# Kernel tuning notes

Measured on AMD Instinct MI355X. Metric: run time of the kernel, lower is better.

The kernel has to match this reference:

```python
import jax, jax.numpy as jnp
import numpy as np
import math

B, S, STATE, H, D = 4, 2048, 1024, 16, 64
N_ROT = 32  # int(0.5*64), even
ROPE_BASE = 10000.0


def setup_inputs() -> dict:
    key = jax.random.key(0)
    ks = jax.random.split(key, 8)
    q_src = jax.random.normal(ks[0], (B, S, STATE), jnp.float32)
    k_src = jax.random.normal(ks[1], (B, S, STATE), jnp.float32)
    v_src = jax.random.normal(ks[2], (B, S, STATE), jnp.float32)
    # causal position mask: True = masked (torch masked_fill semantics)
    position_mask = jnp.triu(jnp.ones((S, S), jnp.bool_), k=1)
    sd = 0.02
    Wq = jax.random.normal(ks[3], (H * D, STATE), jnp.float32) * sd
    Wk = jax.random.normal(ks[4], (H * D, STATE), jnp.float32) * sd
    Wv = jax.random.normal(ks[5], (H * D, STATE), jnp.float32) * sd
    Wo = jax.random.normal(ks[6], (STATE, H * D), jnp.float32) * sd
    return {"q_src": q_src, "k_src": k_src, "v_src": v_src,
            "position_mask": position_mask,
            "Wq": Wq, "Wk": Wk, "Wv": Wv, "Wo": Wo}


def _rotate_half(x):
    x1, x2 = jnp.split(x, 2, axis=-1)
    return jnp.concatenate([-x2, x1], axis=-1)


def _rope(q, k, offset):
    # q,k: [B,H,S,N_ROT]; positions: k at arange(Sk), q at offset+arange(Sq)
    inv_freq = 1.0 / (ROPE_BASE ** (jnp.arange(0, N_ROT, 2, dtype=jnp.float32) / N_ROT))
    def sincos(pos):
        freqs = pos[:, None] * inv_freq[None, :]          # [S, N_ROT/2]
        emb = jnp.concatenate([freqs, freqs], axis=-1)    # [S, N_ROT]
        return jnp.sin(emb), jnp.cos(emb)
    sk, ck = sincos(jnp.arange(k.shape[-2], dtype=jnp.float32))
    sq, cq = sincos(offset + jnp.arange(q.shape[-2], dtype=jnp.float32))
    q = q * cq + _rotate_half(q) * sq
    k = k * ck + _rotate_half(k) * sk
    return q, k


def reference(q_src, k_src, v_src, position_mask, Wq, Wk, Wv, Wo):
    qk_scale = (1.0 / math.sqrt(D)) ** 0.5  # sqrt of 1/sqrt(D), applied to q and k
    def heads(x):  # [B,S,H*D] -> [B,H,S,D]
        return x.reshape(B, S, H, D).transpose(0, 2, 1, 3)
    q = heads((q_src @ Wq.T) * qk_scale)
    k = heads((k_src @ Wk.T) * qk_scale)
    v = heads(v_src @ Wv.T)
    # inline RoPE on first N_ROT dims (pos_offset = 0, no kv cache)
    rq, rk = _rope(q[..., :N_ROT], k[..., :N_ROT], 0.0)
    q = jnp.concatenate([rq, q[..., N_ROT:]], axis=-1)
    k = jnp.concatenate([rk, k[..., N_ROT:]], axis=-1)
    att = jnp.einsum('bhqd,bhkd->bhqk', q, k)
    att = jnp.where(position_mask[None, None], -jnp.inf, att)
    att = jax.nn.softmax(att, axis=-1)
    out = jnp.einsum('bhqk,bhkd->bhqd', att, v)
    out = out.transpose(0, 2, 1, 3).reshape(B, S, H * D)
    return out @ Wo.T
```

## Files before the change

kernel.cpp:

```cpp
#include <hip/hip_runtime.h>

typedef unsigned short u16;
typedef unsigned int u32;
typedef short short8 __attribute__((ext_vector_type(8)));
typedef float f32x4 __attribute__((ext_vector_type(4)));
typedef float f32x16 __attribute__((ext_vector_type(16)));

#define NB 4
#define NS 2048
#define NSTATE 1024
#define NH 16
#define ND 64
#define NM (NB*NS)

#if __has_builtin(__builtin_amdgcn_exp2f)
#define EXP2(x) __builtin_amdgcn_exp2f(x)
#else
#define EXP2(x) __expf((x) * 0.6931471805599453f)
#endif

__device__ __forceinline__ u16 f2bf(float f){
  union { float fv; unsigned uv; } x; x.fv = f;
  unsigned r = x.uv + 0x7fffu + ((x.uv >> 16) & 1u);
  return (u16)(r >> 16);
}

__device__ __forceinline__ u32 cvtpk(float lo, float hi){
  u32 r;
  asm("v_cvt_pk_bf16_f32 %0, %1, %2" : "=v"(r) : "v"(lo), "v"(hi));
  return r;
}

__device__ __forceinline__ f32x4 mfma16x16(short8 a, short8 b, f32x4 c){
  return __builtin_amdgcn_mfma_f32_16x16x32_bf16(a, b, c, 0, 0, 0);
}

__device__ __forceinline__ f32x16 mfma32(short8 a, short8 b, f32x16 c){
  return __builtin_amdgcn_mfma_f32_32x32x16_bf16(a, b, c, 0, 0, 0);
}

__device__ __forceinline__ void gld_lds16(const u16* g, u16* l){
  __builtin_amdgcn_global_load_lds((const __attribute__((address_space(1))) void*)g,
                                   (__attribute__((address_space(3))) void*)l, 16, 0, 0);
}

__global__ __launch_bounds__(256)
void cvt_all(const float* __restrict__ q, const float* __restrict__ k, const float* __restrict__ v,
             const float* __restrict__ wq, const float* __restrict__ wk,
             const float* __restrict__ wv, const float* __restrict__ wo,
             u16* oq, u16* ok, u16* ov, u16* owq, u16* owk, u16* owv, u16* owo){
  const int XN4 = (NB*NS*NSTATE)/4;
  const int WN4 = (NSTATE*NSTATE)/4;
  int gid = blockIdx.x * 256 + threadIdx.x;
  const float* src; u16* dst; int idx;
  if (gid < XN4)          { src = q; dst = oq; idx = gid; }
  else if (gid < 2*XN4)   { src = k; dst = ok; idx = gid - XN4; }
  else if (gid < 3*XN4)   { src = v; dst = ov; idx = gid - 2*XN4; }
  else {
    int g = gid - 3*XN4;
    int wsel = g >> 18;
    idx = g & (WN4 - 1);
    src = (wsel==0)?wq:(wsel==1)?wk:(wsel==2)?wv:wo;
    dst = (wsel==0)?owq:(wsel==1)?owk:(wsel==2)?owv:owo;
  }
  float4 val = ((const float4*)src)[idx];
  ushort4 r;
  r.x = f2bf(val.x); r.y = f2bf(val.y); r.z = f2bf(val.z); r.w = f2bf(val.w);
  ((ushort4*)dst)[idx] = r;
}

__global__ __launch_bounds__(256)
void gemm_qkv(const u16* __restrict__ xq, const u16* __restrict__ xk,
              const u16* __restrict__ xv, const u16* __restrict__ Wcat,
              u16* __restrict__ Qh, u16* __restrict__ Kk, u16* __restrict__ Vt){
  __shared__ __align__(16) u16 As[128*64];
  __shared__ __align__(16) u16 Bs[128*64];
  const int gblk = blockIdx.x;
  const int wid = (gblk & 7) * 192 + (gblk >> 3);
  const int bx = wid % 24, by = wid / 24;
  const int sel = bx >> 3;
  const u16* A = (sel==0) ? xq : (sel==1) ? xk : xv;
  const int tid = threadIdx.x;
  const int lane = tid & 63, w = tid >> 6;
  const int wr = w >> 1, wc = w & 1;
  const int l15 = lane & 15, lhi = lane >> 4;
  const int brow = by * 128;
  const int bcol = bx * 128;
  const int K = NSTATE;
  f32x4 acc[4][4] = {};

  for (int kt = 0; kt < K; kt += 64){
    #pragma unroll
    for (int it = 0; it < 4; ++it){
      int flat = it*4096 + tid*16;
      int row = flat >> 7;
      int cb  = (flat >> 4) & 7;
      int scb = cb ^ (row & 7);
      gld_lds16(A + (size_t)(brow+row)*K + kt + scb*8, As + (flat>>1));
    }
    #pragma unroll
    for (int it = 0; it < 4; ++it){
      int flat = it*4096 + tid*16;
      int row = flat >> 7;
      int cb  = (flat >> 4) & 7;
      int scb = cb ^ (row & 7);
      gld_lds16(Wcat + (size_t)(bcol+row)*K + kt + scb*8, Bs + (flat>>1));
    }
    __syncthreads();
    #pragma unroll
    for (int ks = 0; ks < 2; ++ks){
      short8 av[4], bv[4];
      #pragma unroll
      for (int i = 0; i < 4; ++i){
        int row = wr*64 + i*16 + l15;
        av[i] = *(const short8*)&As[row*64 + (((ks*4 + lhi) ^ (row & 7))*8)];
      }
      #pragma unroll
      for (int j = 0; j < 4; ++j){
        int row = wc*64 + j*16 + l15;
        bv[j] = *(const short8*)&Bs[row*64 + (((ks*4 + lhi) ^ (row & 7))*8)];
      }
      __builtin_amdgcn_s_setprio(1);
      #pragma unroll
      for (int i = 0; i < 4; ++i)
        #pragma unroll
        for (int j = 0; j < 4; ++j)
          acc[i][j] = mfma16x16(av[i], bv[j], acc[i][j]);
      __builtin_amdgcn_s_setprio(0);
    }
    __syncthreads();
  }

  const int col0 = bcol + wc*64;
  if (sel == 2){
    const int head = (col0 & 1023) >> 6;
    #pragma unroll
    for (int i = 0; i < 4; ++i){
      int m0 = brow + wr*64 + i*16 + lhi*4;
      int b = m0 >> 11, s0 = m0 & (NS-1);
      u16* obase = Vt + ((size_t)((b*NH + head)*ND))*NS + s0;
      #pragma unroll
      for (int j = 0; j < 4; ++j){
        int d = j*16 + l15;
        uint2 pk;
        pk.x = cvtpk(acc[i][j][0], acc[i][j][1]);
        pk.y = cvtpk(acc[i][j][2], acc[i][j][3]);
        *(uint2*)(obase + (size_t)d*NS) = pk;
      }
    }
  } else {
    u16* out = sel ? Kk : Qh;
    const float qk_scale = 0.4246609f;
    const int head = (col0 & 1023) >> 6;
    const float invf = EXP2(-0.83048202f * (float)l15);
    #pragma unroll
    for (int i = 0; i < 4; ++i){
      #pragma unroll
      for (int reg = 0; reg < 4; ++reg){
        int m = brow + wr*64 + i*16 + lhi*4 + reg;
        int b = m >> 11, s = m & (NS-1);
        float sn, cs;
        __sincosf((float)s * invf, &sn, &cs);
        float x0 = acc[i][0][reg]*qk_scale;
        float x1 = acc[i][1][reg]*qk_scale;
        u16* orow = out + ((size_t)(b*NH + head)*NS + s)*ND;
        orow[ 0 + l15] = f2bf(x0*cs - x1*sn);
        orow[16 + l15] = f2bf(x1*cs + x0*sn);
        orow[32 + l15] = f2bf(acc[i][2][reg]*qk_scale);
        orow[48 + l15] = f2bf(acc[i][3][reg]*qk_scale);
      }
    }
  }
}

__global__ __launch_bounds__(256)
void gemm_wo(const u16* __restrict__ A, const u16* __restrict__ Bt, float* __restrict__ out){
  __shared__ __align__(16) u16 As[128*64];
  __shared__ __align__(16) u16 Bs[128*64];
  const int gblk = blockIdx.x;
  const int wid = (gblk & 7) * 64 + (gblk >> 3);
  const int bx = wid & 7, by = wid >> 3;
  const int tid = threadIdx.x;
  const int lane = tid & 63, w = tid >> 6;
  const int wr = w >> 1, wc = w & 1;
  const int l15 = lane & 15, lhi = lane >> 4;
  const int brow = by * 128;
  const int bcol = bx * 128;
  const int K = NSTATE;
  f32x4 acc[4][4] = {};

  for (int kt = 0; kt < K; kt += 64){
    #pragma unroll
    for (int it = 0; it < 4; ++it){
      int flat = it*4096 + tid*16;
      int row = flat >> 7;
      int cb  = (flat >> 4) & 7;
      int scb = cb ^ (row & 7);
      gld_lds16(A + (size_t)(brow+row)*K + kt + scb*8, As + (flat>>1));
    }
    #pragma unroll
    for (int it = 0; it < 4; ++it){
      int flat = it*4096 + tid*16;
      int row = flat >> 7;
      int cb  = (flat >> 4) & 7;
      int scb = cb ^ (row & 7);
      gld_lds16(Bt + (size_t)(bcol+row)*K + kt + scb*8, Bs + (flat>>1));
    }
    __syncthreads();
    #pragma unroll
    for (int ks = 0; ks < 2; ++ks){
      short8 av[4], bv[4];
      #pragma unroll
      for (int i = 0; i < 4; ++i){
        int row = wr*64 + i*16 + l15;
        av[i] = *(const short8*)&As[row*64 + (((ks*4 + lhi) ^ (row & 7))*8)];
      }
      #pragma unroll
      for (int j = 0; j < 4; ++j){
        int row = wc*64 + j*16 + l15;
        bv[j] = *(const short8*)&Bs[row*64 + (((ks*4 + lhi) ^ (row & 7))*8)];
      }
      __builtin_amdgcn_s_setprio(1);
      #pragma unroll
      for (int i = 0; i < 4; ++i)
        #pragma unroll
        for (int j = 0; j < 4; ++j)
          acc[i][j] = mfma16x16(av[i], bv[j], acc[i][j]);
      __builtin_amdgcn_s_setprio(0);
    }
    __syncthreads();
  }
  #pragma unroll
  for (int i = 0; i < 4; ++i)
    #pragma unroll
    for (int reg = 0; reg < 4; ++reg){
      int m = brow + wr*64 + i*16 + lhi*4 + reg;
      float* orow = out + (size_t)m*NSTATE + bcol + wc*64;
      #pragma unroll
      for (int j = 0; j < 4; ++j)
        orow[j*16 + l15] = acc[i][j][reg];
    }
}

__global__ __launch_bounds__(256)
void flash_attn(const u16* __restrict__ Q, const u16* __restrict__ Kh,
                const u16* __restrict__ Vt, u16* __restrict__ O){
  __shared__ __align__(16) u16 Kbuf[2][64*64];
  __shared__ __align__(16) u16 Vbuf[2][64*64];
  const int gblk = blockIdx.x;
  const int xcd = gblk & 7, gr = gblk >> 3;
  const int bh  = xcd*8 + (gr & 7);
  const int g   = 15 - (gr >> 3);
  const int tid = threadIdx.x;
  const int w = tid >> 6, lane = tid & 63;
  const int l31 = lane & 31, hi = lane >> 5;
  const u16* Qb = Q  + (size_t)bh*NS*ND;
  const u16* Kb = Kh + (size_t)bh*NS*ND;
  const u16* Vb = Vt + (size_t)bh*ND*NS;
  const int b = bh >> 4, h = bh & 15;
  const int qw = g*128 + w*32;
  const int kend_w   = qw + 32;
  const int kend_blk = g*128 + 128;

  short8 qf[4];
  #pragma unroll
  for (int dd = 0; dd < 4; ++dd)
    qf[dd] = *(const short8*)&Qb[(size_t)(qw + l31)*ND + dd*16 + hi*8];

  f32x16 oacc[2] = {};
  float mrun = 8.0f, lrun = 0.f;

  int cur = 0;
  #pragma unroll
  for (int i = 0; i < 2; ++i){
    int ch = i*256 + tid;
    int row = ch >> 3, cc = ch & 7;
    int scc = cc ^ (row & 7);
    gld_lds16(Kb + (size_t)row*ND + scc*8, &Kbuf[cur][ch*8]);
    gld_lds16(Vb + (size_t)row*NS + scc*8, &Vbuf[cur][ch*8]);
  }
  __syncthreads();

  #pragma unroll 1
  for (int kv0 = 0; kv0 < kend_blk; kv0 += 64){
    if (kv0 + 64 < kend_blk){
      #pragma unroll
      for (int i = 0; i < 2; ++i){
        int ch = i*256 + tid;
        int row = ch >> 3, cc = ch & 7;
        int scc = cc ^ (row & 7);
        gld_lds16(Kb + (size_t)(kv0 + 64 + row)*ND + scc*8, &Kbuf[cur^1][ch*8]);
        gld_lds16(Vb + (size_t)row*NS + kv0 + 64 + scc*8, &Vbuf[cur^1][ch*8]);
      }
    }
    if (kv0 < kend_w){
      const char* kb = (const char*)&Kbuf[cur][0];
      const char* vb = (const char*)&Vbuf[cur][0];
      short8 kf[8];
      #pragma unroll
      for (int kh2 = 0; kh2 < 2; ++kh2)
        #pragma unroll
        for (int dd = 0; dd < 4; ++dd){
          int srow = kh2*32 + l31;
          int off = (srow*128 + dd*32 + hi*16) ^ ((srow & 7) << 4);
          kf[kh2*4+dd] = *(const short8*)(kb + off);
        }
      f32x16 st0 = {}, st1 = {};
      __builtin_amdgcn_s_setprio(1);
      #pragma unroll
      for (int dd = 0; dd < 4; ++dd) st0 = mfma32(kf[dd],   qf[dd], st0);
      #pragma unroll
      for (int dd = 0; dd < 4; ++dd) st1 = mfma32(kf[4+dd], qf[dd], st1);
      __builtin_amdgcn_s_setprio(0);
      if (kv0 + 63 > qw){
        int q = qw + l31;
        #pragma unroll
        for (int r2 = 0; r2 < 16; ++r2){
          int k0 = kv0 + (r2 & 3) + 8*(r2 >> 2) + 4*hi;
          if (k0      > q) st0[r2] = -3.0e30f;
          if (k0 + 32 > q) st1[r2] = -3.0e30f;
        }
      }
      float m0 = fmaxf(fmaxf(st0[0], st0[1]), fmaxf(st0[2], st0[3]));
      float m1 = fmaxf(fmaxf(st0[4], st0[5]), fmaxf(st0[6], st0[7]));
      float m2 = fmaxf(fmaxf(st0[8], st0[9]), fmaxf(st0[10], st0[11]));
      float m3 = fmaxf(fmaxf(st0[12], st0[13]), fmaxf(st0[14], st0[15]));
      float m4 = fmaxf(fmaxf(st1[0], st1[1]), fmaxf(st1[2], st1[3]));
      float m5 = fmaxf(fmaxf(st1[4], st1[5]), fmaxf(st1[6], st1[7]));
      float m6 = fmaxf(fmaxf(st1[8], st1[9]), fmaxf(st1[10], st1[11]));
      float m7 = fmaxf(fmaxf(st1[12], st1[13]), fmaxf(st1[14], st1[15]));
      float pm = fmaxf(fmaxf(fmaxf(m0, m1), fmaxf(m2, m3)),
                       fmaxf(fmaxf(m4, m5), fmaxf(m6, m7)));
      pm = fmaxf(pm, __shfl_xor(pm, 32));
      #pragma unroll
      for (int r2 = 0; r2 < 16; ++r2){
        st0[r2] = EXP2(st0[r2] - mrun);
        st1[r2] = EXP2(st1[r2] - mrun);
      }
      float s0 = 0.f, s1 = 0.f, s2 = 0.f, s3 = 0.f;
      #pragma unroll
      for (int r2 = 0; r2 < 16; r2 += 4){
        s0 += st0[r2+0] + st1[r2+0];
        s1 += st0[r2+1] + st1[r2+1];
        s2 += st0[r2+2] + st1[r2+2];
        s3 += st0[r2+3] + st1[r2+3];
      }
      float rs = (s0 + s1) + (s2 + s3);
      rs += __shfl_xor(rs, 32);
      if (__any(pm > mrun)){
        float mn = fmaxf(mrun, pm);
        float a  = EXP2(mrun - mn);
        mrun = mn;
        lrun = (lrun + rs) * a;
        #pragma unroll
        for (int r2 = 0; r2 < 16; ++r2){
          st0[r2] *= a; st1[r2] *= a;
          oacc[0][r2] *= a; oacc[1][r2] *= a;
        }
      } else {
        lrun += rs;
      }
      short8 paf[4];
      #pragma unroll
      for (int sl = 0; sl < 4; ++sl){
        const f32x16& S = (sl < 2) ? st0 : st1;
        const int base = (sl & 1) * 8;
        u32 a0 = cvtpk(S[base+0], S[base+1]);
        u32 b0 = cvtpk(S[base+4], S[base+5]);
        asm("v_permlane32_swap_b32 %0, %1" : "+v"(a0), "+v"(b0));
        u32 a1 = cvtpk(S[base+2], S[base+3]);
        u32 b1 = cvtpk(S[base+6], S[base+7]);
        asm("v_permlane32_swap_b32 %0, %1" : "+v"(a1), "+v"(b1));
        union { u32 u[4]; short8 v; } pk_;
        pk_.u[0] = a0; pk_.u[1] = a1; pk_.u[2] = b0; pk_.u[3] = b1;
        paf[sl] = pk_.v;
      }
      #pragma unroll
      for (int dh = 0; dh < 2; ++dh){
        short8 vv[4];
        #pragma unroll
        for (int sl = 0; sl < 4; ++sl){
          int drow = dh*32 + l31;
          int off = (drow*128 + sl*32 + hi*16) ^ ((drow & 7) << 4);
          vv[sl] = *(const short8*)(vb + off);
        }
        __builtin_amdgcn_s_setprio(1);
        #pragma unroll
        for (int sl = 0; sl < 4; ++sl)
          oacc[dh] = mfma32(vv[sl], paf[sl], oacc[dh]);
        __builtin_amdgcn_s_setprio(0);
      }
    }
    __syncthreads();
    cur ^= 1;
  }

  float inv = 1.0f / lrun;
  u16* orow = O + ((size_t)(b*NS + qw + l31))*NSTATE + h*ND;
  #pragma unroll
  for (int dh = 0; dh < 2; ++dh)
    #pragma unroll
    for (int rq = 0; rq < 4; ++rq){
      uint2 pk;
      pk.x = cvtpk(oacc[dh][rq*4+0]*inv, oacc[dh][rq*4+1]*inv);
      pk.y = cvtpk(oacc[dh][rq*4+2]*inv, oacc[dh][rq*4+3]*inv);
      *(uint2*)(orow + dh*32 + rq*8 + hi*4) = pk;
    }
}

extern "C" void kernel_launch(void* const* d_in, const int* in_sizes, int n_in,
                              void* d_out, int out_size, void* d_ws, size_t ws_size,
                              hipStream_t stream){
  const float* q_src = (const float*)d_in[0];
  const float* k_src = (const float*)d_in[1];
  const float* v_src = (const float*)d_in[2];
  const float* Wq = (const float*)d_in[4];
  const float* Wk = (const float*)d_in[5];
  const float* Wv = (const float*)d_in[6];
  const float* Wo = (const float*)d_in[7];

  char* ws = (char*)d_ws;
  const size_t MB = 1u << 20;
  if (ws_size < 104*MB) return;

  u16* xq   = (u16*)(ws +  0*MB);
  u16* xk   = (u16*)(ws + 16*MB);
  u16* xv   = (u16*)(ws + 32*MB);
  u16* wq16 = (u16*)(ws + 48*MB);
  u16* wk16 = (u16*)(ws + 50*MB);
  u16* wv16 = (u16*)(ws + 52*MB);
  u16* wo16 = (u16*)(ws + 54*MB);
  u16* Qh   = (u16*)(ws + 56*MB);
  u16* Kk   = (u16*)(ws + 72*MB);
  u16* Vt   = (u16*)(ws + 88*MB);
  u16* Oat  = xk;

  cvt_all<<<dim3(28672), dim3(256), 0, stream>>>(q_src, k_src, v_src, Wq, Wk, Wv, Wo,
                                                 xq, xk, xv, wq16, wk16, wv16, wo16);
  gemm_qkv<<<dim3(1536), dim3(256), 0, stream>>>(xq, xk, xv, wq16, Qh, Kk, Vt);
  flash_attn<<<dim3(1024), dim3(256), 0, stream>>>(Qh, Kk, Vt, Oat);
  gemm_wo<<<dim3(512), dim3(256), 0, stream>>>(Oat, wo16, (float*)d_out);
}
```

Baseline: 196.3 us.

## Pair causal q-tiles per block and compute softmax row sums via MFMA

Each flash-attention block now handles two q-tiles, c and 15-c, one after the other, so every block does an equal share of the causal work, and the grid is halved to 512. The softmax denominator is no longer built from a VALU reduction plus cross-lane shuffle. Instead it comes from an extra MFMA of a bf16 ones vector against the probability fragments, and the max reduction uses 3-input max. These are meant to remove load imbalance and tail effects across causal blocks and to cut VALU work per tile. In exchange each block runs longer, fewer blocks are resident, four MFMAs are added per tile, and the row sum is now taken from bf16-rounded probabilities.

Result: no change. 192.7 us (-1.9%).

```diff
diff --git a/kernel.cpp b/kernel.cpp
--- a/kernel.cpp
+++ b/kernel.cpp
@@ -29,6 +29,10 @@
   u32 r;
   asm("v_cvt_pk_bf16_f32 %0, %1, %2" : "=v"(r) : "v"(lo), "v"(hi));
   return r;
+}
+
+__device__ __forceinline__ float max3f(float a, float b, float c){
+  return fmaxf(fmaxf(a, b), c);
 }
 
 __device__ __forceinline__ f32x4 mfma16x16(short8 a, short8 b, f32x4 c){
@@ -250,7 +254,7 @@
   const int gblk = blockIdx.x;
   const int xcd = gblk & 7, gr = gblk >> 3;
   const int bh  = xcd*8 + (gr & 7);
-  const int g   = 15 - (gr >> 3);
+  const int c   = gr >> 3;
   const int tid = threadIdx.x;
   const int w = tid >> 6, lane = tid & 63;
   const int l31 = lane & 31, hi = lane >> 5;
@@ -258,154 +262,162 @@
   const u16* Kb = Kh + (size_t)bh*NS*ND;
   const u16* Vb = Vt + (size_t)bh*ND*NS;
   const int b = bh >> 4, h = bh & 15;
-  const int qw = g*128 + w*32;
-  const int kend_w   = qw + 32;
-  const int kend_blk = g*128 + 128;
-
-  short8 qf[4];
+
+  short8 ones;
   #pragma unroll
-  for (int dd = 0; dd < 4; ++dd)
-    qf[dd] = *(const short8*)&Qb[(size_t)(qw + l31)*ND + dd*16 + hi*8];
-
-  f32x16 oacc[2] = {};
-  float mrun = 8.0f, lrun = 0.f;
-
-  int cur = 0;
-  #pragma unroll
-  for (int i = 0; i < 2; ++i){
-    int ch = i*256 + tid;
-    int row = ch >> 3, cc = ch & 7;
-    int scc = cc ^ (row & 7);
-    gld_lds16(Kb + (size_t)row*ND + scc*8, &Kbuf[cur][ch*8]);
-    gld_lds16(Vb + (size_t)row*NS + scc*8, &Vbuf[cur][ch*8]);
+  for (int i = 0; i < 8; ++i) ones[i] = (short)0x3F80;
+
+  #pragma unroll 1
+  for (int ph = 0; ph < 2; ++ph){
+    const int g  = ph ? (15 - c) : c;
+    const int qw = g*128 + w*32;
+    const int kend_w   = qw + 32;
+    const int kend_blk = g*128 + 128;
+
+    short8 qf[4];
+    #pragma unroll
+    for (int dd = 0; dd < 4; ++dd)
+      qf[dd] = *(const short8*)&Qb[(size_t)(qw + l31)*ND + dd*16 + hi*8];
+
+    f32x16 oacc[2] = {};
+    f32x16 lacc = {};
+    float mrun = 12.0f;
+
+    int cur = 0;
+    #pragma unroll
+    for (int i = 0; i < 2; ++i){
+      int ch = i*256 + tid;
+      int row = ch >> 3, cc = ch & 7;
+      int scc = cc ^ (row & 7);
+      gld_lds16(Kb + (size_t)row*ND + scc*8, &Kbuf[cur][ch*8]);
+      gld_lds16(Vb + (size_t)row*NS + scc*8, &Vbuf[cur][ch*8]);
+    }
+    __syncthreads();
+
+    #pragma unroll 1
+    for (int kv0 = 0; kv0 < kend_blk; kv0 += 64){
+      if (kv0 + 64 < kend_blk){
+        #pragma unroll
+        for (int i = 0; i < 2; ++i){
+          int ch = i*256 + tid;
+          int row = ch >> 3, cc = ch & 7;
+          int scc = cc ^ (row & 7);
+          gld_lds16(Kb + (size_t)(kv0 + 64 + row)*ND + scc*8, &Kbuf[cur^1][ch*8]);
+          gld_lds16(Vb + (size_t)row*NS + kv0 + 64 + scc*8, &Vbuf[cur^1][ch*8]);
+        }
+      }
+      if (kv0 < kend_w){
+        const char* kb = (const char*)&Kbuf[cur][0];
+        const char* vb = (const char*)&Vbuf[cur][0];
+        short8 kf[8];
+        #pragma unroll
+        for (int kh2 = 0; kh2 < 2; ++kh2)
+          #pragma unroll
+          for (int dd = 0; dd < 4; ++dd){
+            int srow = kh2*32 + l31;
+            int off = (srow*128 + dd*32 + hi*16) ^ ((srow & 7) << 4);
+            kf[kh2*4+dd] = *(const short8*)(kb + off);
+          }
+        f32x16 st0 = {}, st1 = {};
+        __builtin_amdgcn_s_setprio(1);
+        #pragma unroll
+        for (int dd = 0; dd < 4; ++dd) st0 = mfma32(kf[dd],   qf[dd], st0);
+        #pragma unroll
+        for (int dd = 0; dd < 4; ++dd) st1 = mfma32(kf[4+dd], qf[dd], st1);
+        __builtin_amdgcn_s_setprio(0);
+        if (kv0 + 63 > qw){
+          int q = qw + l31;
+          #pragma unroll
+          for (int r2 = 0; r2 < 16; ++r2){
+            int k0 = kv0 + (r2 & 3) + 8*(r2 >> 2) + 4*hi;
+            if (k0      > q) st0[r2] = -3.0e30f;
+            if (k0 + 32 > q) st1[r2] = -3.0e30f;
+          }
+        }
+        float t0 = max3f(st0[0],  st0[1],  st0[2]);
+        float t1 = max3f(st0[3],  st0[4],  st0[5]);
+        float t2 = max3f(st0[6],  st0[7],  st0[8]);
+        float t3 = max3f(st0[9],  st0[10], st0[11]);
+        float t4 = max3f(st0[12], st0[13], st0[14]);
+        float t5 = max3f(st1[0],  st1[1],  st1[2]);
+        float t6 = max3f(st1[3],  st1[4],  st1[5]);
+        float t7 = max3f(st1[6],  st1[7],  st1[8]);
+        float t8 = max3f(st1[9],  st1[10], st1[11]);
+        float t9 = max3f(st1[12], st1[13], st1[14]);
+        float u0 = max3f(t0, t1, t2);
+        float u1 = max3f(t3, t4, st0[15]);
+        float u2 = max3f(t5, t6, t7);
+        float u3 = max3f(t8, t9, st1[15]);
+        float pm = fmaxf(max3f(u0, u1, u2), u3);
+        pm = fmaxf(pm, __shfl_xor(pm, 32));
+        #pragma unroll
+        for (int r2 = 0; r2 < 16; ++r2){
+          st0[r2] = EXP2(st0[r2] - mrun);
+          st1[r2] = EXP2(st1[r2] - mrun);
+        }
+        if (__any(pm > mrun)){
+          float mn = fmaxf(mrun, pm);
+          float a  = EXP2(mrun - mn);
+          mrun = mn;
+          #pragma unroll
+          for (int r2 = 0; r2 < 16; ++r2){
+            st0[r2] *= a; st1[r2] *= a;
+            oacc[0][r2] *= a; oacc[1][r2] *= a;
+            lacc[r2] *= a;
+          }
+        }
+        short8 paf[4];
+        #pragma unroll
+        for (int sl = 0; sl < 4; ++sl){
+          const f32x16& S = (sl < 2) ? st0 : st1;
+          const int base = (sl & 1) * 8;
+          u32 a0 = cvtpk(S[base+0], S[base+1]);
+          u32 b0 = cvtpk(S[base+4], S[base+5]);
+          asm("v_permlane32_swap_b32 %0, %1" : "+v"(a0), "+v"(b0));
+          u32 a1 = cvtpk(S[base+2], S[base+3]);
+          u32 b1 = cvtpk(S[base+6], S[base+7]);
+          asm("v_permlane32_swap_b32 %0, %1" : "+v"(a1), "+v"(b1));
+          union { u32 u[4]; short8 v; } pk_;
+          pk_.u[0] = a0; pk_.u[1] = a1; pk_.u[2] = b0; pk_.u[3] = b1;
+          paf[sl] = pk_.v;
+        }
+        #pragma unroll
+        for (int dh = 0; dh < 2; ++dh){
+          short8 vv[4];
+          #pragma unroll
+          for (int sl = 0; sl < 4; ++sl){
+            int drow = dh*32 + l31;
+            int off = (drow*128 + sl*32 + hi*16) ^ ((drow & 7) << 4);
+            vv[sl] = *(const short8*)(vb + off);
+          }
+          __builtin_amdgcn_s_setprio(1);
+          #pragma unroll
+          for (int sl = 0; sl < 4; ++sl)
+            oacc[dh] = mfma32(vv[sl], paf[sl], oacc[dh]);
+          __builtin_amdgcn_s_setprio(0);
+        }
+        __builtin_amdgcn_s_setprio(1);
+        #pragma unroll
+        for (int sl = 0; sl < 4; ++sl)
+          lacc = mfma32(ones, paf[sl], lacc);
+        __builtin_amdgcn_s_setprio(0);
+      }
+      __syncthreads();
+      cur ^= 1;
+    }
+
+    float inv = 1.0f / lacc[0];
+    u16* orow = O + ((size_t)(b*NS + qw + l31))*NSTATE + h*ND;
+    #pragma unroll
+    for (int dh = 0; dh < 2; ++dh)
+      #pragma unroll
+      for (int rq = 0; rq < 4; ++rq){
+        uint2 pk;
+        pk.x = cvtpk(oacc[dh][rq*4+0]*inv, oacc[dh][rq*4+1]*inv);
+        pk.y = cvtpk(oacc[dh][rq*4+2]*inv, oacc[dh][rq*4+3]*inv);
+        *(uint2*)(orow + dh*32 + rq*8 + hi*4) = pk;
+      }
   }
-  __syncthreads();
-
-  #pragma unroll 1
-  for (int kv0 = 0; kv0 < kend_blk; kv0 += 64){
-    if (kv0 + 64 < kend_blk){
-      #pragma unroll
-      for (int i = 0; i < 2; ++i){
-        int ch = i*256 + tid;
-        int row = ch >> 3, cc = ch & 7;
-        int scc = cc ^ (row & 7);
-        gld_lds16(Kb + (size_t)(kv0 + 64 + row)*ND + scc*8, &Kbuf[cur^1][ch*8]);
-        gld_lds16(Vb + (size_t)row*NS + kv0 + 64 + scc*8, &Vbuf[cur^1][ch*8]);
-      }
-    }
-    if (kv0 < kend_w){
-      const char* kb = (const char*)&Kbuf[cur][0];
-      const char* vb = (const char*)&Vbuf[cur][0];
-      short8 kf[8];
-      #pragma unroll
-      for (int kh2 = 0; kh2 < 2; ++kh2)
-        #pragma unroll
-        for (int dd = 0; dd < 4; ++dd){
-          int srow = kh2*32 + l31;
-          int off = (srow*128 + dd*32 + hi*16) ^ ((srow & 7) << 4);
-          kf[kh2*4+dd] = *(const short8*)(kb + off);
-        }
-      f32x16 st0 = {}, st1 = {};
-      __builtin_amdgcn_s_setprio(1);
-      #pragma unroll
-      for (int dd = 0; dd < 4; ++dd) st0 = mfma32(kf[dd],   qf[dd], st0);
-      #pragma unroll
-      for (int dd = 0; dd < 4; ++dd) st1 = mfma32(kf[4+dd], qf[dd], st1);
-      __builtin_amdgcn_s_setprio(0);
-      if (kv0 + 63 > qw){
-        int q = qw + l31;
-        #pragma unroll
-        for (int r2 = 0; r2 < 16; ++r2){
-          int k0 = kv0 + (r2 & 3) + 8*(r2 >> 2) + 4*hi;
-          if (k0      > q) st0[r2] = -3.0e30f;
-          if (k0 + 32 > q) st1[r2] = -3.0e30f;
-        }
-      }
-      float m0 = fmaxf(fmaxf(st0[0], st0[1]), fmaxf(st0[2], st0[3]));
-      float m1 = fmaxf(fmaxf(st0[4], st0[5]), fmaxf(st0[6], st0[7]));
-      float m2 = fmaxf(fmaxf(st0[8], st0[9]), fmaxf(st0[10], st0[11]));
-      float m3 = fmaxf(fmaxf(st0[12], st0[13]), fmaxf(st0[14], st0[15]));
-      float m4 = fmaxf(fmaxf(st1[0], st1[1]), fmaxf(st1[2], st1[3]));
-      float m5 = fmaxf(fmaxf(st1[4], st1[5]), fmaxf(st1[6], st1[7]));
-      float m6 = fmaxf(fmaxf(st1[8], st1[9]), fmaxf(st1[10], st1[11]));
-      float m7 = fmaxf(fmaxf(st1[12], st1[13]), fmaxf(st1[14], st1[15]));
-      float pm = fmaxf(fmaxf(fmaxf(m0, m1), fmaxf(m2, m3)),
-                       fmaxf(fmaxf(m4, m5), fmaxf(m6, m7)));
-      pm = fmaxf(pm, __shfl_xor(pm, 32));
-      #pragma unroll
-      for (int r2 = 0; r2 < 16; ++r2){
-        st0[r2] = EXP2(st0[r2] - mrun);
-        st1[r2] = EXP2(st1[r2] - mrun);
-      }
-      float s0 = 0.f, s1 = 0.f, s2 = 0.f, s3 = 0.f;
-      #pragma unroll
-      for (int r2 = 0; r2 < 16; r2 += 4){
-        s0 += st0[r2+0] + st1[r2+0];
-        s1 += st0[r2+1] + st1[r2+1];
-        s2 += st0[r2+2] + st1[r2+2];
-        s3 += st0[r2+3] + st1[r2+3];
-      }
-      float rs = (s0 + s1) + (s2 + s3);
-      rs += __shfl_xor(rs, 32);
-      if (__any(pm > mrun)){
-        float mn = fmaxf(mrun, pm);
-        float a  = EXP2(mrun - mn);
-        mrun = mn;
-        lrun = (lrun + rs) * a;
-        #pragma unroll
-        for (int r2 = 0; r2 < 16; ++r2){
-          st0[r2] *= a; st1[r2] *= a;
-          oacc[0][r2] *= a; oacc[1][r2] *= a;
-        }
-      } else {
-        lrun += rs;
-      }
-      short8 paf[4];
-      #pragma unroll
-      for (int sl = 0; sl < 4; ++sl){
-        const f32x16& S = (sl < 2) ? st0 : st1;
-        const int base = (sl & 1) * 8;
-        u32 a0 = cvtpk(S[base+0], S[base+1]);
-        u32 b0 = cvtpk(S[base+4], S[base+5]);
-        asm("v_permlane32_swap_b32 %0, %1" : "+v"(a0), "+v"(b0));
-        u32 a1 = cvtpk(S[base+2], S[base+3]);
-        u32 b1 = cvtpk(S[base+6], S[base+7]);
-        asm("v_permlane32_swap_b32 %0, %1" : "+v"(a1), "+v"(b1));
-        union { u32 u[4]; short8 v; } pk_;
-        pk_.u[0] = a0; pk_.u[1] = a1; pk_.u[2] = b0; pk_.u[3] = b1;
-        paf[sl] = pk_.v;
-      }
-      #pragma unroll
-      for (int dh = 0; dh < 2; ++dh){
-        short8 vv[4];
-        #pragma unroll
-        for (int sl = 0; sl < 4; ++sl){
-          int drow = dh*32 + l31;
-          int off = (drow*128 + sl*32 + hi*16) ^ ((drow & 7) << 4);
-          vv[sl] = *(const short8*)(vb + off);
-        }
-        __builtin_amdgcn_s_setprio(1);
-        #pragma unroll
-        for (int sl = 0; sl < 4; ++sl)
-          oacc[dh] = mfma32(vv[sl], paf[sl], oacc[dh]);
-        __builtin_amdgcn_s_setprio(0);
-      }
-    }
-    __syncthreads();
-    cur ^= 1;
-  }
-
-  float inv = 1.0f / lrun;
-  u16* orow = O + ((size_t)(b*NS + qw + l31))*NSTATE + h*ND;
-  #pragma unroll
-  for (int dh = 0; dh < 2; ++dh)
-    #pragma unroll
-    for (int rq = 0; rq < 4; ++rq){
-      uint2 pk;
-      pk.x = cvtpk(oacc[dh][rq*4+0]*inv, oacc[dh][rq*4+1]*inv);
-      pk.y = cvtpk(oacc[dh][rq*4+2]*inv, oacc[dh][rq*4+3]*inv);
-      *(uint2*)(orow + dh*32 + rq*8 + hi*4) = pk;
-    }
 }
 
 extern "C" void kernel_launch(void* const* d_in, const int* in_sizes, int n_in,
@@ -438,6 +450,6 @@
   cvt_all<<<dim3(28672), dim3(256), 0, stream>>>(q_src, k_src, v_src, Wq, Wk, Wv, Wo,
                                                  xq, xk, xv, wq16, wk16, wv16, wo16);
   gemm_qkv<<<dim3(1536), dim3(256), 0, stream>>>(xq, xk, xv, wq16, Qh, Kk, Vt);
-  flash_attn<<<dim3(1024), dim3(256), 0, stream>>>(Qh, Kk, Vt, Oat);
+  flash_attn<<<dim3(512), dim3(256), 0, stream>>>(Qh, Kk, Vt, Oat);
   gemm_wo<<<dim3(512), dim3(256), 0, stream>>>(Oat, wo16, (float*)d_out);
 }
```
